# Performance work log

Measured on AMD Instinct MI355X. Metric: run time of the kernel, lower is better.

Reference implementation:

```python
import jax, jax.numpy as jnp
import numpy as np

BLOCK_SIZE = 32
BLOCK_COUNTS = 4
LENS = np.array([512, 256, 384, 128, 512, 256], dtype=np.int64)  # jagged seq lens, sum = 2048


def _silu(x):
    return x * jax.nn.sigmoid(x)


def _pad_idx(offs, lens, L):
    # gather indices + validity mask to pad a jagged tensor to [B, L, ...]
    i = offs[:-1][:, None] + np.arange(L)[None, :]
    m = np.arange(L)[None, :] < lens[:, None]
    return np.where(m, i, 0), m


def _hstu_bsa_forward(q, k, v, g_cmp, g_slc, offsets):
    offsets = np.asarray(offsets)
    B = offsets.shape[0] - 1
    seq_lens = offsets[1:] - offsets[:-1]
    T, H, D = q.shape
    BS = BLOCK_SIZE
    cmp_lens = (seq_lens + BS - 1) // BS
    offs_cmp = np.concatenate([[0], np.cumsum(cmp_lens)])
    Tc = int(offs_cmp[-1])
    max_n = int(seq_lens.max())
    max_b = int(cmp_lens.max())
    scale = float(D) ** -0.5

    batch_ids = np.repeat(np.arange(B), seq_lens)            # [T]
    local_pos = np.arange(T) - offsets[batch_ids]            # [T]
    seg = jnp.asarray(offs_cmp[batch_ids] + local_pos // BS)  # [T] global cmp segment id

    # --- block mean-pooled compressed K/V (jagged [Tc,H,D]) ---
    k_cmp = jax.ops.segment_sum(k, seg, num_segments=Tc)
    v_cmp = jax.ops.segment_sum(v, seg, num_segments=Tc)
    cnt = jax.ops.segment_sum(jnp.ones((T,), q.dtype), seg, num_segments=Tc)
    cnt = jnp.clip(cnt, 1.0)[:, None, None]
    k_cmp = k_cmp / cnt
    v_cmp = v_cmp / cnt

    # --- pad jagged to dense for compressed attention + selection ---
    qi, qm = _pad_idx(offsets, seq_lens, max_n)   # [B,max_n]
    ci, cm = _pad_idx(offs_cmp, cmp_lens, max_b)  # [B,max_b]
    pq = q[jnp.asarray(qi)] * jnp.asarray(qm)[..., None, None]        # [B,max_n,H,D]
    pkc = k_cmp[jnp.asarray(ci)] * jnp.asarray(cm)[..., None, None]   # [B,max_b,H,D]
    pvc = v_cmp[jnp.asarray(ci)] * jnp.asarray(cm)[..., None, None]

    scores = jnp.einsum('bqhd,bkhd->bhqk', pq, pkc) * scale           # [B,H,max_n,max_b]
    q_blk = np.arange(max_n)[:, None] // BS
    causal = q_blk >= np.arange(max_b)[None, :]                        # query block >= cmp block

    # --- compressed attention (SiLU score fn, no softmax), gated by g_cmp ---
    mask_cmp = jnp.asarray(causal)[None, None] & jnp.asarray(cm)[:, None, None, :]
    p_cmp = jnp.where(mask_cmp, _silu(scores), 0.0)
    o_cmp_pad = jnp.einsum('bhqk,bkhd->bqhd', p_cmp, pvc)
    o_cmp = o_cmp_pad[batch_ids, local_pos] * g_cmp[..., None]         # [T,H,D]

    # --- per-token top-S block selection on compressed scores ---
    S = min(BLOCK_COUNTS, max_b)
    sel_scores = jnp.where(jnp.asarray(causal)[None, None], scores, -jnp.inf)
    _, top_idx = jax.lax.top_k(sel_scores, S)        # [B,H,max_n,S]
    b_idx = top_idx[batch_ids, :, local_pos]         # [T,H,S] (jagged)

    # --- selective block-sparse attention over raw jagged K/V ---
    L = S * BS
    tgt_local = (b_idx[..., None] * BS + jnp.arange(BS)).reshape(T, H, L)
    tgt = jnp.asarray(offsets[batch_ids])[:, None, None] + tgt_local   # global token idx
    cur = jnp.asarray(offsets[batch_ids] + local_pos)[:, None, None]
    is_causal = tgt <= cur                         # also kills non-causal -inf selections
    tgt_c = jnp.clip(tgt, 0, T - 1)
    h_ix = jnp.arange(H)[None, :, None]
    k_g = k[tgt_c, h_ix]                            # [T,H,L,D]
    v_g = v[tgt_c, h_ix]
    s_slc = jnp.einsum('thd,thld->thl', q, k_g) * scale
    p_slc = jnp.where(is_causal, _silu(s_slc), 0.0)
    o_slc = jnp.einsum('thl,thld->thd', p_slc, v_g) * g_slc[..., None]
    return o_cmp, o_slc


def setup_inputs() -> dict:
    key = jax.random.key(0)
    k0, k1, k2, k3, k4 = jax.random.split(key, 5)
    T, H, D = int(LENS.sum()), 4, 64
    offsets = np.concatenate([[0], np.cumsum(LENS)]).astype(np.int64)
    return {
        'q': jax.random.normal(k0, (T, H, D), jnp.float32),
        'k': jax.random.normal(k1, (T, H, D), jnp.float32),
        'v': jax.random.normal(k2, (T, H, D), jnp.float32),
        'g_cmp': jax.random.uniform(k3, (T, H), jnp.float32),
        'g_slc': jax.random.uniform(k4, (T, H), jnp.float32),
        'x_offsets': jnp.asarray(offsets),
    }


def reference(q, k, v, g_cmp, g_slc, x_offsets):
    return _hstu_bsa_forward(q, k, v, g_cmp, g_slc, np.asarray(x_offsets))
```

## Files before the change

### kernel.cpp

```cpp
#include <hip/hip_runtime.h>
#include <math.h>

#define HH 4
#define DD 64
#define BS 32

typedef __attribute__((ext_vector_type(8))) short bf16x8;
typedef __attribute__((ext_vector_type(4))) float f32x4;
#define MFMA16(a,b,c) __builtin_amdgcn_mfma_f32_16x16x32_bf16(a,b,c,0,0,0)

__device__ __forceinline__ float silu_f(float x) { return x / (1.0f + __expf(-x)); }
__device__ __forceinline__ unsigned short f2bf(float f) {
    unsigned u = __float_as_uint(f);
    return (unsigned short)((u + 0x7fffu + ((u >> 16) & 1u)) >> 16);
}

__global__ __launch_bounds__(256) void hstu_prep(
    const float* __restrict__ q, const float* __restrict__ k, const float* __restrict__ v,
    const int* __restrict__ offsets, int B,
    float* __restrict__ k_cmp, float* __restrict__ v_cmp,
    uint4* __restrict__ kbA, uint4* __restrict__ qbB, uint4* __restrict__ vbB,
    int4* __restrict__ cmeta) {
    int c = blockIdx.x, h = blockIdx.y;
    int acc = 0, b = -1, jc = 0;
    for (int bb = 0; bb < B; ++bb) {
        int len = offsets[bb + 1] - offsets[bb];
        int nb = (len + BS - 1) >> 5;
        if (b < 0 && c < acc + nb) { b = bb; jc = c - acc; }
        acc += nb;
    }
    int tid = threadIdx.x, rg = tid >> 6, lane = tid & 63;
    if (b < 0) { if (h == 0 && tid == 0) cmeta[c] = make_int4(-1, -1, 0, 0); return; }
    int t0 = offsets[b] + jc * BS;
    int cnt = offsets[b + 1] - t0; if (cnt > BS) cnt = BS;
    if (h == 0 && tid == 0) cmeta[c] = make_int4(b, jc, t0, cnt);

    __shared__ __align__(16) float kf[BS][DD + 1];
    __shared__ __align__(16) float vf[BS][DD + 1];
    __shared__ __align__(16) unsigned short q16[BS][DD];
    __shared__ float redk[4][DD], redv[4][DD];

    #pragma unroll
    for (int it = 0; it < 2; ++it) {
        int fi = tid + it * 256;
        int row = fi >> 4, ch = fi & 15;
        float4 kk = make_float4(0.f, 0.f, 0.f, 0.f), vv = kk, qq = kk;
        if (row < cnt) {
            size_t off = (size_t)(t0 + row) * (HH * DD) + h * DD + ch * 4;
            kk = *(const float4*)(k + off);
            vv = *(const float4*)(v + off);
            qq = *(const float4*)(q + off);
        }
        kf[row][ch*4+0] = kk.x; kf[row][ch*4+1] = kk.y; kf[row][ch*4+2] = kk.z; kf[row][ch*4+3] = kk.w;
        vf[row][ch*4+0] = vv.x; vf[row][ch*4+1] = vv.y; vf[row][ch*4+2] = vv.z; vf[row][ch*4+3] = vv.w;
        q16[row][ch*4+0] = f2bf(qq.x); q16[row][ch*4+1] = f2bf(qq.y);
        q16[row][ch*4+2] = f2bf(qq.z); q16[row][ch*4+3] = f2bf(qq.w);
    }
    __syncthreads();

    float kp = 0.f, vp = 0.f;
    #pragma unroll
    for (int m = 0; m < 8; ++m) {
        int row = rg * 8 + m;
        kp += kf[row][lane]; vp += vf[row][lane];
    }
    redk[rg][lane] = kp; redv[rg][lane] = vp;
    __syncthreads();

    int l15 = lane & 15, l4 = lane >> 4;
    size_t fb = ((size_t)c * HH + h) * 4;

    if (rg == 0) {
        float inv = 1.0f / (float)cnt;
        float a = (redk[0][lane] + redk[1][lane] + redk[2][lane] + redk[3][lane]) * inv;
        float bb2 = (redv[0][lane] + redv[1][lane] + redv[2][lane] + redv[3][lane]) * inv;
        k_cmp[(size_t)c * (HH * DD) + h * DD + lane] = a;
        v_cmp[(size_t)c * (HH * DD) + h * DD + lane] = bb2;
    } else if (rg == 1) {
        #pragma unroll
        for (int mt = 0; mt < 2; ++mt) {
            int row = mt * 16 + l15;
            #pragma unroll
            for (int hf = 0; hf < 2; ++hf) {
                int d0 = hf * 32 + l4 * 8;
                unsigned w0 = (unsigned)f2bf(kf[row][d0+0]) | ((unsigned)f2bf(kf[row][d0+1]) << 16);
                unsigned w1 = (unsigned)f2bf(kf[row][d0+2]) | ((unsigned)f2bf(kf[row][d0+3]) << 16);
                unsigned w2 = (unsigned)f2bf(kf[row][d0+4]) | ((unsigned)f2bf(kf[row][d0+5]) << 16);
                unsigned w3 = (unsigned)f2bf(kf[row][d0+6]) | ((unsigned)f2bf(kf[row][d0+7]) << 16);
                uint4 o = {w0, w1, w2, w3};
                kbA[(fb + mt * 2 + hf) * 64 + lane] = o;
            }
        }
    } else if (rg == 2) {
        #pragma unroll
        for (int nt = 0; nt < 2; ++nt) {
            int tok = nt * 16 + l15;
            #pragma unroll
            for (int ks2 = 0; ks2 < 2; ++ks2) {
                int d0 = ks2 * 32 + l4 * 8;
                qbB[(fb + nt * 2 + ks2) * 64 + lane] = *(const uint4*)&q16[tok][d0];
            }
        }
    } else {
        #pragma unroll
        for (int dt = 0; dt < 4; ++dt) {
            int d = dt * 16 + l15;
            int kr = l4 * 8;
            unsigned w0 = (unsigned)f2bf(vf[kr+0][d]) | ((unsigned)f2bf(vf[kr+1][d]) << 16);
            unsigned w1 = (unsigned)f2bf(vf[kr+2][d]) | ((unsigned)f2bf(vf[kr+3][d]) << 16);
            unsigned w2 = (unsigned)f2bf(vf[kr+4][d]) | ((unsigned)f2bf(vf[kr+5][d]) << 16);
            unsigned w3 = (unsigned)f2bf(vf[kr+6][d]) | ((unsigned)f2bf(vf[kr+7][d]) << 16);
            uint4 o = {w0, w1, w2, w3};
            vbB[(fb + dt) * 64 + lane] = o;
        }
    }
}

__global__ __launch_bounds__(256) void hstu_sel(
    const float* __restrict__ q, const float* __restrict__ g_cmp,
    const int* __restrict__ offsets, int B,
    const float* __restrict__ k_cmp, const float* __restrict__ v_cmp,
    float* __restrict__ o_cmp, unsigned short* __restrict__ selmask) {
    int t = blockIdx.x;
    int h = threadIdx.x >> 6;
    int lane = threadIdx.x & 63;
    __shared__ __align__(16) float s_lds[HH][16];
    __shared__ __align__(16) float p_lds[HH][16];

    int b = 0;
    while (b + 1 < B && t >= offsets[b + 1]) ++b;
    int p = t - offsets[b];
    int q_blk = p >> 5;
    int base_cmp = 0, totC = 0;
    for (int bb = 0; bb < B; ++bb) {
        int nb = (offsets[bb + 1] - offsets[bb] + BS - 1) >> 5;
        if (bb < b) base_cmp += nb;
        totC += nb;
    }

    int d4 = lane & 15, c4 = lane >> 4;
    float4 qf = *(const float4*)(q + ((size_t)t * HH + h) * DD + d4 * 4);
    float sc_own[4], pc_own[4];
    #pragma unroll
    for (int m = 0; m < 4; ++m) {
        int j = m * 4 + c4;
        int ci = base_cmp + j; if (ci > totC - 1) ci = totC - 1;
        float4 kk = *(const float4*)(k_cmp + (size_t)ci * (HH * DD) + h * DD + d4 * 4);
        float pp = qf.x * kk.x + qf.y * kk.y + qf.z * kk.z + qf.w * kk.w;
        pp += __shfl_xor(pp, 1);
        pp += __shfl_xor(pp, 2);
        pp += __shfl_xor(pp, 4);
        pp += __shfl_xor(pp, 8);
        sc_own[m] = pp * 0.125f;
        pc_own[m] = (j <= q_blk) ? silu_f(sc_own[m]) : 0.f;
    }
    if (d4 == 0) {
        #pragma unroll
        for (int m = 0; m < 4; ++m) {
            s_lds[h][m * 4 + c4] = sc_own[m];
            p_lds[h][m * 4 + c4] = pc_own[m];
        }
    }
    __builtin_amdgcn_wave_barrier();

    float sc_[16], pc_[16];
    #pragma unroll
    for (int x = 0; x < 4; ++x) {
        float4 sd = ((const float4*)s_lds[h])[x];
        float4 pd = ((const float4*)p_lds[h])[x];
        sc_[x*4+0] = sd.x; sc_[x*4+1] = sd.y; sc_[x*4+2] = sd.z; sc_[x*4+3] = sd.w;
        pc_[x*4+0] = pd.x; pc_[x*4+1] = pd.y; pc_[x*4+2] = pd.z; pc_[x*4+3] = pd.w;
    }

    int j_own = lane >> 2;
    float s_own = sc_[j_own];
    int rank = 0;
    #pragma unroll
    for (int kk = 0; kk < 16; ++kk) {
        bool beats = (kk <= q_blk) && ((sc_[kk] > s_own) || (sc_[kk] == s_own && kk < j_own));
        rank += beats ? 1 : 0;
    }
    bool mine = ((lane & 3) == 0) && (j_own <= q_blk) && (rank < 4);
    unsigned long long msk = __ballot(mine);
    unsigned selm = 0;
    #pragma unroll
    for (int jj2 = 0; jj2 < 16; ++jj2)
        selm |= ((unsigned)((msk >> (4 * jj2)) & 1ull)) << jj2;
    if (lane == 0) selmask[(size_t)t * HH + h] = (unsigned short)selm;

    float4 facc = make_float4(0.f, 0.f, 0.f, 0.f);
    #pragma unroll
    for (int m = 0; m < 4; ++m) {
        int j = m * 4 + c4;
        int ci = base_cmp + j; if (ci > totC - 1) ci = totC - 1;
        float4 vv = *(const float4*)(v_cmp + (size_t)ci * (HH * DD) + h * DD + d4 * 4);
        float pj = pc_[j];
        facc.x += pj * vv.x; facc.y += pj * vv.y; facc.z += pj * vv.z; facc.w += pj * vv.w;
    }
    facc.x += __shfl_xor(facc.x, 16); facc.x += __shfl_xor(facc.x, 32);
    facc.y += __shfl_xor(facc.y, 16); facc.y += __shfl_xor(facc.y, 32);
    facc.z += __shfl_xor(facc.z, 16); facc.z += __shfl_xor(facc.z, 32);
    facc.w += __shfl_xor(facc.w, 16); facc.w += __shfl_xor(facc.w, 32);
    if (c4 == 0) {
        float gc = g_cmp[(size_t)t * HH + h];
        float4 o = make_float4(facc.x * gc, facc.y * gc, facc.z * gc, facc.w * gc);
        *(float4*)(o_cmp + ((size_t)t * HH + h) * DD + d4 * 4) = o;
    }
}

__global__ __launch_bounds__(256) void hstu_slc_mfma(
    const float* __restrict__ g_slc,
    const uint4* __restrict__ kbA, const uint4* __restrict__ qbB, const uint4* __restrict__ vbB,
    const int4* __restrict__ cmeta, const unsigned short* __restrict__ selmask,
    float* __restrict__ o_slc) {
    int c = blockIdx.x, h = blockIdx.y;
    int4 meta = cmeta[c];
    int jc = meta.y;
    if (jc < 0) return;
    int t0_blk = meta.z, cnt = meta.w;
    int base_c = c - jc;

    int tid = threadIdx.x, w = tid >> 6, lane = tid & 63;
    int l15 = lane & 15, l4 = lane >> 4;

    __shared__ __align__(16) unsigned short plds[4][BS * BS];
    __shared__ __align__(16) float red[4][BS][DD];

    unsigned sm_l = 0;
    if (lane < BS && lane < cnt)
        sm_l = (unsigned)selmask[(size_t)(t0_blk + lane) * HH + h];
    unsigned sm_n0 = __shfl(sm_l, l15);
    unsigned sm_n1 = __shfl(sm_l, 16 + l15);

    size_t qfb = ((size_t)c * HH + h) * 4;
    uint4 qb0 = qbB[(qfb + 0) * 64 + lane], qb1 = qbB[(qfb + 1) * 64 + lane];
    uint4 qb2 = qbB[(qfb + 2) * 64 + lane], qb3 = qbB[(qfb + 3) * 64 + lane];

    f32x4 z = {0.f, 0.f, 0.f, 0.f};
    f32x4 oacc[2][4];
    #pragma unroll
    for (int tt = 0; tt < 2; ++tt)
        #pragma unroll
        for (int dt = 0; dt < 4; ++dt) oacc[tt][dt] = z;

    int jcb = jc * BS;
    for (int jj = w; jj <= jc; jj += 4) {
        if (__ballot((sm_l >> jj) & 1u) == 0ull) continue;
        size_t kfb = ((size_t)(base_c + jj) * HH + h) * 4;
        uint4 ka00 = kbA[(kfb + 0) * 64 + lane], ka01 = kbA[(kfb + 1) * 64 + lane];
        uint4 ka10 = kbA[(kfb + 2) * 64 + lane], ka11 = kbA[(kfb + 3) * 64 + lane];
        uint4 vb0 = vbB[(kfb + 0) * 64 + lane], vb1 = vbB[(kfb + 1) * 64 + lane];
        uint4 vb2 = vbB[(kfb + 2) * 64 + lane], vb3 = vbB[(kfb + 3) * 64 + lane];

        f32x4 sq[2][2];
        sq[0][0] = MFMA16(*(bf16x8*)&ka00, *(bf16x8*)&qb0, z);
        sq[0][0] = MFMA16(*(bf16x8*)&ka01, *(bf16x8*)&qb1, sq[0][0]);
        sq[0][1] = MFMA16(*(bf16x8*)&ka00, *(bf16x8*)&qb2, z);
        sq[0][1] = MFMA16(*(bf16x8*)&ka01, *(bf16x8*)&qb3, sq[0][1]);
        sq[1][0] = MFMA16(*(bf16x8*)&ka10, *(bf16x8*)&qb0, z);
        sq[1][0] = MFMA16(*(bf16x8*)&ka11, *(bf16x8*)&qb1, sq[1][0]);
        sq[1][1] = MFMA16(*(bf16x8*)&ka10, *(bf16x8*)&qb2, z);
        sq[1][1] = MFMA16(*(bf16x8*)&ka11, *(bf16x8*)&qb3, sq[1][1]);

        int jjb = jj * BS;
        #pragma unroll
        for (int mt = 0; mt < 2; ++mt) {
            #pragma unroll
            for (int nt = 0; nt < 2; ++nt) {
                int tokl = nt * 16 + l15;
                unsigned sm = nt ? sm_n1 : sm_n0;
                bool selb = (sm >> jj) & 1u;
                #pragma unroll
                for (int i = 0; i < 4; ++i) {
                    int krl = mt * 16 + l4 * 4 + i;
                    bool mk = selb && (jjb + krl <= jcb + tokl);
                    float ps = mk ? silu_f(sq[mt][nt][i] * 0.125f) : 0.f;
                    plds[w][tokl * BS + (((krl >> 3) ^ ((tokl >> 1) & 3)) << 3) + (krl & 7)] = f2bf(ps);
                }
            }
        }
        __builtin_amdgcn_wave_barrier();
        #pragma unroll
        for (int tt = 0; tt < 2; ++tt) {
            int tokl = tt * 16 + l15;
            uint4 pu = *(const uint4*)&plds[w][tokl * BS + ((l4 ^ ((tokl >> 1) & 3)) << 3)];
            bf16x8 pa = *(bf16x8*)&pu;
            oacc[tt][0] = MFMA16(pa, *(bf16x8*)&vb0, oacc[tt][0]);
            oacc[tt][1] = MFMA16(pa, *(bf16x8*)&vb1, oacc[tt][1]);
            oacc[tt][2] = MFMA16(pa, *(bf16x8*)&vb2, oacc[tt][2]);
            oacc[tt][3] = MFMA16(pa, *(bf16x8*)&vb3, oacc[tt][3]);
        }
        __builtin_amdgcn_wave_barrier();
    }

    #pragma unroll
    for (int tt = 0; tt < 2; ++tt)
        #pragma unroll
        for (int dt = 0; dt < 4; ++dt)
            #pragma unroll
            for (int i = 0; i < 4; ++i)
                red[w][tt * 16 + l4 * 4 + i][dt * 16 + l15] = oacc[tt][dt][i];
    __syncthreads();
    #pragma unroll
    for (int it = 0; it < 2; ++it) {
        int job = tid + it * 256;
        int tok = job >> 4, ch = job & 15;
        if (tok < cnt) {
            float4 a0 = *(const float4*)&red[0][tok][ch * 4];
            float4 a1 = *(const float4*)&red[1][tok][ch * 4];
            float4 a2 = *(const float4*)&red[2][tok][ch * 4];
            float4 a3 = *(const float4*)&red[3][tok][ch * 4];
            float gs = g_slc[(size_t)(t0_blk + tok) * HH + h];
            float4 o = make_float4((a0.x + a1.x + a2.x + a3.x) * gs,
                                   (a0.y + a1.y + a2.y + a3.y) * gs,
                                   (a0.z + a1.z + a2.z + a3.z) * gs,
                                   (a0.w + a1.w + a2.w + a3.w) * gs);
            *(float4*)(o_slc + ((size_t)(t0_blk + tok) * HH + h) * DD + ch * 4) = o;
        }
    }
}

extern "C" void kernel_launch(void* const* d_in, const int* in_sizes, int n_in,
                              void* d_out, int out_size, void* d_ws, size_t ws_size,
                              hipStream_t stream) {
    const float* q     = (const float*)d_in[0];
    const float* k     = (const float*)d_in[1];
    const float* v     = (const float*)d_in[2];
    const float* g_cmp = (const float*)d_in[3];
    const float* g_slc = (const float*)d_in[4];
    const int*   offs  = (const int*)d_in[5];

    int T = in_sizes[0] / (HH * DD);
    int B = in_sizes[5] - 1;
    int maxC = (T + BS - 1) / BS + B;

    char* w = (char*)d_ws;
    uint4* kbA = (uint4*)w;  w += (size_t)maxC * HH * 4 * 64 * sizeof(uint4);
    uint4* qbB = (uint4*)w;  w += (size_t)maxC * HH * 4 * 64 * sizeof(uint4);
    uint4* vbB = (uint4*)w;  w += (size_t)maxC * HH * 4 * 64 * sizeof(uint4);
    int4*  cmeta = (int4*)w; w += (size_t)maxC * sizeof(int4);
    float* k_cmp = (float*)w; w += (size_t)maxC * HH * DD * sizeof(float);
    float* v_cmp = (float*)w; w += (size_t)maxC * HH * DD * sizeof(float);
    unsigned short* selmask = (unsigned short*)w;

    float* o_cmp = (float*)d_out;
    float* o_slc = (float*)d_out + (size_t)T * HH * DD;

    hipLaunchKernelGGL(hstu_prep, dim3(maxC, HH), dim3(256), 0, stream,
                       q, k, v, offs, B, k_cmp, v_cmp, kbA, qbB, vbB, cmeta);
    hipLaunchKernelGGL(hstu_sel, dim3(T), dim3(256), 0, stream,
                       q, g_cmp, offs, B, k_cmp, v_cmp, o_cmp, selmask);
    hipLaunchKernelGGL(hstu_slc_mfma, dim3(maxC, HH), dim3(256), 0, stream,
                       g_slc, kbA, qbB, vbB, cmeta, selmask, o_slc);
}
```

Before: 28.88 us.

## Fuse selection kernel into MFMA selected-attention kernel per compressed block

Merges the per-token top-k selection and compressed attention kernel into the per-block MFMA selection kernel. The selection mask now lives in LDS instead of global memory, and the bf16 Q fragments are built in-kernel from an LDS copy of Q instead of being staged by the prep kernel. This drops one kernel launch and the global round trips for selmask and qbB. The cost is fewer, heavier blocks for the compressed-attention part (maxC*H blocks instead of T blocks) and more LDS use per block, which may reduce occupancy.

```diff
diff --git a/kernel.cpp b/kernel.cpp
--- a/kernel.cpp
+++ b/kernel.cpp
@@ -16,10 +16,10 @@
 }
 
 __global__ __launch_bounds__(256) void hstu_prep(
-    const float* __restrict__ q, const float* __restrict__ k, const float* __restrict__ v,
+    const float* __restrict__ k, const float* __restrict__ v,
     const int* __restrict__ offsets, int B,
     float* __restrict__ k_cmp, float* __restrict__ v_cmp,
-    uint4* __restrict__ kbA, uint4* __restrict__ qbB, uint4* __restrict__ vbB,
+    uint4* __restrict__ kbA, uint4* __restrict__ vbB,
     int4* __restrict__ cmeta) {
     int c = blockIdx.x, h = blockIdx.y;
     int acc = 0, b = -1, jc = 0;
@@ -37,24 +37,20 @@
 
     __shared__ __align__(16) float kf[BS][DD + 1];
     __shared__ __align__(16) float vf[BS][DD + 1];
-    __shared__ __align__(16) unsigned short q16[BS][DD];
     __shared__ float redk[4][DD], redv[4][DD];
 
     #pragma unroll
     for (int it = 0; it < 2; ++it) {
         int fi = tid + it * 256;
         int row = fi >> 4, ch = fi & 15;
-        float4 kk = make_float4(0.f, 0.f, 0.f, 0.f), vv = kk, qq = kk;
+        float4 kk = make_float4(0.f, 0.f, 0.f, 0.f), vv = kk;
         if (row < cnt) {
             size_t off = (size_t)(t0 + row) * (HH * DD) + h * DD + ch * 4;
             kk = *(const float4*)(k + off);
             vv = *(const float4*)(v + off);
-            qq = *(const float4*)(q + off);
         }
         kf[row][ch*4+0] = kk.x; kf[row][ch*4+1] = kk.y; kf[row][ch*4+2] = kk.z; kf[row][ch*4+3] = kk.w;
         vf[row][ch*4+0] = vv.x; vf[row][ch*4+1] = vv.y; vf[row][ch*4+2] = vv.z; vf[row][ch*4+3] = vv.w;
-        q16[row][ch*4+0] = f2bf(qq.x); q16[row][ch*4+1] = f2bf(qq.y);
-        q16[row][ch*4+2] = f2bf(qq.z); q16[row][ch*4+3] = f2bf(qq.w);
     }
     __syncthreads();
 
@@ -92,16 +88,6 @@
             }
         }
     } else if (rg == 2) {
-        #pragma unroll
-        for (int nt = 0; nt < 2; ++nt) {
-            int tok = nt * 16 + l15;
-            #pragma unroll
-            for (int ks2 = 0; ks2 < 2; ++ks2) {
-                int d0 = ks2 * 32 + l4 * 8;
-                qbB[(fb + nt * 2 + ks2) * 64 + lane] = *(const uint4*)&q16[tok][d0];
-            }
-        }
-    } else {
         #pragma unroll
         for (int dt = 0; dt < 4; ++dt) {
             int d = dt * 16 + l15;
@@ -116,125 +102,138 @@
     }
 }
 
-__global__ __launch_bounds__(256) void hstu_sel(
-    const float* __restrict__ q, const float* __restrict__ g_cmp,
+__global__ __launch_bounds__(256) void hstu_fused(
+    const float* __restrict__ q,
+    const float* __restrict__ g_cmp, const float* __restrict__ g_slc,
     const int* __restrict__ offsets, int B,
     const float* __restrict__ k_cmp, const float* __restrict__ v_cmp,
-    float* __restrict__ o_cmp, unsigned short* __restrict__ selmask) {
-    int t = blockIdx.x;
-    int h = threadIdx.x >> 6;
-    int lane = threadIdx.x & 63;
-    __shared__ __align__(16) float s_lds[HH][16];
-    __shared__ __align__(16) float p_lds[HH][16];
-
-    int b = 0;
-    while (b + 1 < B && t >= offsets[b + 1]) ++b;
-    int p = t - offsets[b];
-    int q_blk = p >> 5;
-    int base_cmp = 0, totC = 0;
-    for (int bb = 0; bb < B; ++bb) {
-        int nb = (offsets[bb + 1] - offsets[bb] + BS - 1) >> 5;
-        if (bb < b) base_cmp += nb;
-        totC += nb;
-    }
-
-    int d4 = lane & 15, c4 = lane >> 4;
-    float4 qf = *(const float4*)(q + ((size_t)t * HH + h) * DD + d4 * 4);
-    float sc_own[4], pc_own[4];
-    #pragma unroll
-    for (int m = 0; m < 4; ++m) {
-        int j = m * 4 + c4;
-        int ci = base_cmp + j; if (ci > totC - 1) ci = totC - 1;
-        float4 kk = *(const float4*)(k_cmp + (size_t)ci * (HH * DD) + h * DD + d4 * 4);
-        float pp = qf.x * kk.x + qf.y * kk.y + qf.z * kk.z + qf.w * kk.w;
-        pp += __shfl_xor(pp, 1);
-        pp += __shfl_xor(pp, 2);
-        pp += __shfl_xor(pp, 4);
-        pp += __shfl_xor(pp, 8);
-        sc_own[m] = pp * 0.125f;
-        pc_own[m] = (j <= q_blk) ? silu_f(sc_own[m]) : 0.f;
-    }
-    if (d4 == 0) {
-        #pragma unroll
-        for (int m = 0; m < 4; ++m) {
-            s_lds[h][m * 4 + c4] = sc_own[m];
-            p_lds[h][m * 4 + c4] = pc_own[m];
-        }
-    }
-    __builtin_amdgcn_wave_barrier();
-
-    float sc_[16], pc_[16];
-    #pragma unroll
-    for (int x = 0; x < 4; ++x) {
-        float4 sd = ((const float4*)s_lds[h])[x];
-        float4 pd = ((const float4*)p_lds[h])[x];
-        sc_[x*4+0] = sd.x; sc_[x*4+1] = sd.y; sc_[x*4+2] = sd.z; sc_[x*4+3] = sd.w;
-        pc_[x*4+0] = pd.x; pc_[x*4+1] = pd.y; pc_[x*4+2] = pd.z; pc_[x*4+3] = pd.w;
-    }
-
-    int j_own = lane >> 2;
-    float s_own = sc_[j_own];
-    int rank = 0;
-    #pragma unroll
-    for (int kk = 0; kk < 16; ++kk) {
-        bool beats = (kk <= q_blk) && ((sc_[kk] > s_own) || (sc_[kk] == s_own && kk < j_own));
-        rank += beats ? 1 : 0;
-    }
-    bool mine = ((lane & 3) == 0) && (j_own <= q_blk) && (rank < 4);
-    unsigned long long msk = __ballot(mine);
-    unsigned selm = 0;
-    #pragma unroll
-    for (int jj2 = 0; jj2 < 16; ++jj2)
-        selm |= ((unsigned)((msk >> (4 * jj2)) & 1ull)) << jj2;
-    if (lane == 0) selmask[(size_t)t * HH + h] = (unsigned short)selm;
-
-    float4 facc = make_float4(0.f, 0.f, 0.f, 0.f);
-    #pragma unroll
-    for (int m = 0; m < 4; ++m) {
-        int j = m * 4 + c4;
-        int ci = base_cmp + j; if (ci > totC - 1) ci = totC - 1;
-        float4 vv = *(const float4*)(v_cmp + (size_t)ci * (HH * DD) + h * DD + d4 * 4);
-        float pj = pc_[j];
-        facc.x += pj * vv.x; facc.y += pj * vv.y; facc.z += pj * vv.z; facc.w += pj * vv.w;
-    }
-    facc.x += __shfl_xor(facc.x, 16); facc.x += __shfl_xor(facc.x, 32);
-    facc.y += __shfl_xor(facc.y, 16); facc.y += __shfl_xor(facc.y, 32);
-    facc.z += __shfl_xor(facc.z, 16); facc.z += __shfl_xor(facc.z, 32);
-    facc.w += __shfl_xor(facc.w, 16); facc.w += __shfl_xor(facc.w, 32);
-    if (c4 == 0) {
-        float gc = g_cmp[(size_t)t * HH + h];
-        float4 o = make_float4(facc.x * gc, facc.y * gc, facc.z * gc, facc.w * gc);
-        *(float4*)(o_cmp + ((size_t)t * HH + h) * DD + d4 * 4) = o;
-    }
-}
-
-__global__ __launch_bounds__(256) void hstu_slc_mfma(
-    const float* __restrict__ g_slc,
-    const uint4* __restrict__ kbA, const uint4* __restrict__ qbB, const uint4* __restrict__ vbB,
-    const int4* __restrict__ cmeta, const unsigned short* __restrict__ selmask,
-    float* __restrict__ o_slc) {
+    const uint4* __restrict__ kbA, const uint4* __restrict__ vbB,
+    const int4* __restrict__ cmeta,
+    float* __restrict__ o_cmp, float* __restrict__ o_slc) {
     int c = blockIdx.x, h = blockIdx.y;
     int4 meta = cmeta[c];
     int jc = meta.y;
     if (jc < 0) return;
     int t0_blk = meta.z, cnt = meta.w;
-    int base_c = c - jc;
-
-    int tid = threadIdx.x, w = tid >> 6, lane = tid & 63;
-    int l15 = lane & 15, l4 = lane >> 4;
-
+    int base_cmp = c - jc;
+    int nc = jc + 1;
+
+    __shared__ __align__(16) float4 qls[BS * 17];
+    __shared__ __align__(16) float4 kcl[16 * 16];
+    __shared__ __align__(16) float4 vcl[16 * 16];
     __shared__ __align__(16) unsigned short plds[4][BS * BS];
     __shared__ __align__(16) float red[4][BS][DD];
-
-    unsigned sm_l = 0;
-    if (lane < BS && lane < cnt)
-        sm_l = (unsigned)selmask[(size_t)(t0_blk + lane) * HH + h];
+    __shared__ __align__(16) float s_scr[4][16];
+    __shared__ __align__(16) float p_scr[4][16];
+    __shared__ unsigned selmask_lds[BS];
+
+    int tid = threadIdx.x;
+    for (int idx = tid; idx < BS * 16; idx += 256) {
+        int row = idx >> 4, ch = idx & 15;
+        float4 z4 = make_float4(0.f, 0.f, 0.f, 0.f);
+        qls[row * 17 + ch] = (row < cnt)
+            ? *(const float4*)(q + (size_t)(t0_blk + row) * (HH * DD) + h * DD + ch * 4) : z4;
+    }
+    for (int idx = tid; idx < nc * 16; idx += 256) {
+        int j = idx >> 4, i = idx & 15;
+        size_t g = (size_t)(base_cmp + j) * (HH * DD) + h * DD + i * 4;
+        int d = j * 16 + (i ^ (j & 7));
+        kcl[d] = *(const float4*)(k_cmp + g);
+        vcl[d] = *(const float4*)(v_cmp + g);
+    }
+    if (tid < BS) selmask_lds[tid] = 0;
+    __syncthreads();
+
+    int w = tid >> 6, lane = tid & 63;
+    int l15 = lane & 15, l4 = lane >> 4;
+
+    {
+        int j16 = lane >> 2, g4 = lane & 3;
+        int c4 = lane >> 4, d4 = lane & 15;
+        for (int m = 0; m < 8; ++m) {
+            int tok = w + m * 4;
+            if (tok >= cnt) continue;
+            int t = t0_blk + tok;
+            int jclp = (j16 < nc) ? j16 : nc - 1;
+            float pp = 0.f;
+            #pragma unroll
+            for (int cc2 = 0; cc2 < 4; ++cc2) {
+                float4 qv = qls[tok * 17 + g4 * 4 + cc2];
+                float4 kk = kcl[jclp * 16 + ((g4 * 4 + cc2) ^ (jclp & 7))];
+                pp += qv.x * kk.x + qv.y * kk.y + qv.z * kk.z + qv.w * kk.w;
+            }
+            pp += __shfl_xor(pp, 1);
+            pp += __shfl_xor(pp, 2);
+            float s_sc = pp * 0.125f;
+            float p_sc = (j16 < nc) ? silu_f(s_sc) : 0.f;
+            if (g4 == 0) { s_scr[w][j16] = s_sc; p_scr[w][j16] = p_sc; }
+            __builtin_amdgcn_wave_barrier();
+            float sc_[16], pc_[16];
+            #pragma unroll
+            for (int x = 0; x < 4; ++x) {
+                float4 sd = ((const float4*)s_scr[w])[x];
+                float4 pd = ((const float4*)p_scr[w])[x];
+                sc_[4*x] = sd.x; sc_[4*x+1] = sd.y; sc_[4*x+2] = sd.z; sc_[4*x+3] = sd.w;
+                pc_[4*x] = pd.x; pc_[4*x+1] = pd.y; pc_[4*x+2] = pd.z; pc_[4*x+3] = pd.w;
+            }
+            float s_own = sc_[j16];
+            int rank = 0;
+            #pragma unroll
+            for (int kx = 0; kx < 16; ++kx) {
+                bool beats = (kx < nc) && ((sc_[kx] > s_own) || (sc_[kx] == s_own && kx < j16));
+                rank += beats ? 1 : 0;
+            }
+            bool mine = (g4 == 0) && (j16 < nc) && (rank < 4);
+            unsigned long long msk = __ballot(mine);
+            unsigned selm = 0;
+            #pragma unroll
+            for (int jj2 = 0; jj2 < 16; ++jj2)
+                selm |= ((unsigned)((msk >> (4 * jj2)) & 1ull)) << jj2;
+            if (lane == 0) selmask_lds[tok] = selm;
+            float4 facc = make_float4(0.f, 0.f, 0.f, 0.f);
+            #pragma unroll
+            for (int m2 = 0; m2 < 4; ++m2) {
+                int jj = m2 * 4 + c4;
+                int jjc = (jj < nc) ? jj : nc - 1;
+                float4 vv = vcl[jjc * 16 + (d4 ^ (jjc & 7))];
+                float pj = pc_[jj];
+                facc.x += pj * vv.x; facc.y += pj * vv.y;
+                facc.z += pj * vv.z; facc.w += pj * vv.w;
+            }
+            facc.x += __shfl_xor(facc.x, 16); facc.x += __shfl_xor(facc.x, 32);
+            facc.y += __shfl_xor(facc.y, 16); facc.y += __shfl_xor(facc.y, 32);
+            facc.z += __shfl_xor(facc.z, 16); facc.z += __shfl_xor(facc.z, 32);
+            facc.w += __shfl_xor(facc.w, 16); facc.w += __shfl_xor(facc.w, 32);
+            if (c4 == 0) {
+                float gc = g_cmp[(size_t)t * HH + h];
+                float4 o = make_float4(facc.x * gc, facc.y * gc, facc.z * gc, facc.w * gc);
+                *(float4*)(o_cmp + ((size_t)t * HH + h) * DD + d4 * 4) = o;
+            }
+        }
+    }
+    __syncthreads();
+
+    bf16x8 qb[2][2];
+    #pragma unroll
+    for (int nt = 0; nt < 2; ++nt) {
+        int tokl = nt * 16 + l15;
+        #pragma unroll
+        for (int ks2 = 0; ks2 < 2; ++ks2) {
+            int d0 = ks2 * 32 + l4 * 8;
+            float4 f0 = qls[tokl * 17 + (d0 >> 2)];
+            float4 f1 = qls[tokl * 17 + (d0 >> 2) + 1];
+            bf16x8 a;
+            a[0] = (short)f2bf(f0.x); a[1] = (short)f2bf(f0.y);
+            a[2] = (short)f2bf(f0.z); a[3] = (short)f2bf(f0.w);
+            a[4] = (short)f2bf(f1.x); a[5] = (short)f2bf(f1.y);
+            a[6] = (short)f2bf(f1.z); a[7] = (short)f2bf(f1.w);
+            qb[nt][ks2] = a;
+        }
+    }
+
+    unsigned sm_l = (lane < BS) ? selmask_lds[lane] : 0u;
     unsigned sm_n0 = __shfl(sm_l, l15);
     unsigned sm_n1 = __shfl(sm_l, 16 + l15);
-
-    size_t qfb = ((size_t)c * HH + h) * 4;
-    uint4 qb0 = qbB[(qfb + 0) * 64 + lane], qb1 = qbB[(qfb + 1) * 64 + lane];
-    uint4 qb2 = qbB[(qfb + 2) * 64 + lane], qb3 = qbB[(qfb + 3) * 64 + lane];
 
     f32x4 z = {0.f, 0.f, 0.f, 0.f};
     f32x4 oacc[2][4];
@@ -246,21 +245,21 @@
     int jcb = jc * BS;
     for (int jj = w; jj <= jc; jj += 4) {
         if (__ballot((sm_l >> jj) & 1u) == 0ull) continue;
-        size_t kfb = ((size_t)(base_c + jj) * HH + h) * 4;
+        size_t kfb = ((size_t)(base_cmp + jj) * HH + h) * 4;
         uint4 ka00 = kbA[(kfb + 0) * 64 + lane], ka01 = kbA[(kfb + 1) * 64 + lane];
         uint4 ka10 = kbA[(kfb + 2) * 64 + lane], ka11 = kbA[(kfb + 3) * 64 + lane];
         uint4 vb0 = vbB[(kfb + 0) * 64 + lane], vb1 = vbB[(kfb + 1) * 64 + lane];
         uint4 vb2 = vbB[(kfb + 2) * 64 + lane], vb3 = vbB[(kfb + 3) * 64 + lane];
 
         f32x4 sq[2][2];
-        sq[0][0] = MFMA16(*(bf16x8*)&ka00, *(bf16x8*)&qb0, z);
-        sq[0][0] = MFMA16(*(bf16x8*)&ka01, *(bf16x8*)&qb1, sq[0][0]);
-        sq[0][1] = MFMA16(*(bf16x8*)&ka00, *(bf16x8*)&qb2, z);
-        sq[0][1] = MFMA16(*(bf16x8*)&ka01, *(bf16x8*)&qb3, sq[0][1]);
-        sq[1][0] = MFMA16(*(bf16x8*)&ka10, *(bf16x8*)&qb0, z);
-        sq[1][0] = MFMA16(*(bf16x8*)&ka11, *(bf16x8*)&qb1, sq[1][0]);
-        sq[1][1] = MFMA16(*(bf16x8*)&ka10, *(bf16x8*)&qb2, z);
-        sq[1][1] = MFMA16(*(bf16x8*)&ka11, *(bf16x8*)&qb3, sq[1][1]);
+        sq[0][0] = MFMA16(*(bf16x8*)&ka00, qb[0][0], z);
+        sq[0][0] = MFMA16(*(bf16x8*)&ka01, qb[0][1], sq[0][0]);
+        sq[0][1] = MFMA16(*(bf16x8*)&ka00, qb[1][0], z);
+        sq[0][1] = MFMA16(*(bf16x8*)&ka01, qb[1][1], sq[0][1]);
+        sq[1][0] = MFMA16(*(bf16x8*)&ka10, qb[0][0], z);
+        sq[1][0] = MFMA16(*(bf16x8*)&ka11, qb[0][1], sq[1][0]);
+        sq[1][1] = MFMA16(*(bf16x8*)&ka10, qb[1][0], z);
+        sq[1][1] = MFMA16(*(bf16x8*)&ka11, qb[1][1], sq[1][1]);
 
         int jjb = jj * BS;
         #pragma unroll
@@ -336,20 +335,16 @@
 
     char* w = (char*)d_ws;
     uint4* kbA = (uint4*)w;  w += (size_t)maxC * HH * 4 * 64 * sizeof(uint4);
-    uint4* qbB = (uint4*)w;  w += (size_t)maxC * HH * 4 * 64 * sizeof(uint4);
     uint4* vbB = (uint4*)w;  w += (size_t)maxC * HH * 4 * 64 * sizeof(uint4);
     int4*  cmeta = (int4*)w; w += (size_t)maxC * sizeof(int4);
     float* k_cmp = (float*)w; w += (size_t)maxC * HH * DD * sizeof(float);
     float* v_cmp = (float*)w; w += (size_t)maxC * HH * DD * sizeof(float);
-    unsigned short* selmask = (unsigned short*)w;
 
     float* o_cmp = (float*)d_out;
     float* o_slc = (float*)d_out + (size_t)T * HH * DD;
 
     hipLaunchKernelGGL(hstu_prep, dim3(maxC, HH), dim3(256), 0, stream,
-                       q, k, v, offs, B, k_cmp, v_cmp, kbA, qbB, vbB, cmeta);
-    hipLaunchKernelGGL(hstu_sel, dim3(T), dim3(256), 0, stream,
-                       q, g_cmp, offs, B, k_cmp, v_cmp, o_cmp, selmask);
-    hipLaunchKernelGGL(hstu_slc_mfma, dim3(maxC, HH), dim3(256), 0, stream,
-                       g_slc, kbA, qbB, vbB, cmeta, selmask, o_slc);
+                       k, v, offs, B, k_cmp, v_cmp, kbA, vbB, cmeta);
+    hipLaunchKernelGGL(hstu_fused, dim3(maxC, HH), dim3(256), 0, stream,
+                       q, g_cmp, g_slc, offs, B, k_cmp, v_cmp, kbA, vbB, cmeta, o_cmp, o_slc);
 }
```

Result: slower. 37.53 us (+29.9%).
